# Kernel optimization log

Measured on AMD Instinct MI355X. Metric: run time of the kernel, lower is better.

## Reference

```python
import jax, jax.numpy as jnp
import numpy as np
from jax import lax

CANTOR_DEPTH = 8
VOCAB, D = 100000, 128


def setup_inputs() -> dict:
    key = jax.random.key(0)
    pentachora = jax.random.normal(key, (VOCAB, 5, D), dtype=jnp.float32)
    return {"pentachora": pentachora}


def _cantor_positions(V):
    # V: [N, 5, D]
    dt = V.dtype
    diff = V[:, :, None, :] - V[:, None, :, :]          # [N,5,5,D]
    dist_sq = jnp.sum(diff * diff, axis=-1)             # [N,5,5]
    N = V.shape[0]

    # Batched 6x6 Cayley-Menger matrix
    M = jnp.zeros((N, 6, 6), dtype=dt)
    M = M.at[:, 0, 1:].set(1.0)
    M = M.at[:, 1:, 0].set(1.0)
    M = M.at[:, 1:, 1:].set(dist_sq)
    det = jnp.linalg.det(M)                              # [N]
    volume = jnp.sqrt(jnp.clip(-det / 9216.0, 0.0))

    # Edge statistics over the 10 unique edges (torch .std() uses ddof=1)
    iu, ju = np.triu_indices(5, k=1)
    edge_lengths = jnp.sqrt(dist_sq[:, iu, ju])          # [N,10]
    mean_edge = jnp.mean(edge_lengths, axis=-1)
    std_edge = jnp.std(edge_lengths, axis=-1, ddof=1)

    # Vertex spread from centroid (ddof=1)
    centroid = jnp.mean(V, axis=1, keepdims=True)        # [N,1,D]
    cdist = jnp.linalg.norm(V - centroid, axis=-1)       # [N,5]
    spread = jnp.std(cdist, axis=-1, ddof=1)

    volume_norm = jax.nn.sigmoid(volume * 10.0)
    edge_ratio = jax.nn.sigmoid(std_edge / (mean_edge + 1e-6))
    spread_norm = jax.nn.sigmoid(spread)

    seed = jnp.clip(volume_norm * 0.4 + edge_ratio * 0.3 + spread_norm * 0.3,
                    1e-6, 1.0 - 1e-6)
    drift = (volume_norm + edge_ratio + spread_norm) * 0.01

    def step(carry, factor):
        x, cv = carry
        x_scaled = x * 3.0
        digit = jnp.floor(x_scaled)                      # x>0 so floor==trunc
        x_frac = x_scaled - digit
        cv = cv + (digit == 2.0).astype(dt) * factor
        x = jnp.clip(x_frac + drift, 1e-6, 1.0 - 1e-6)
        return (x, cv), None

    factors = (0.5 ** jnp.arange(1, CANTOR_DEPTH + 1)).astype(dt)
    (_, cantor_val), _ = lax.scan(step, (seed, jnp.zeros_like(seed)), factors)
    return jnp.clip(cantor_val, 0.0, 1.0)                # [N]


def reference(pentachora):
    return _cantor_positions(pentachora)
```

## Files before the change

kernel.cpp:

```cpp
#include <hip/hip_runtime.h>
#include <math.h>


__device__ __forceinline__ constexpr int gidx(int i, int j) {
    return i * 5 - i * (i - 1) / 2 + (j - i);
}

__global__ __launch_bounds__(256, 4) void fingerprint_kernel(
    const float* __restrict__ pent, float* __restrict__ out, int nItems)
{
    __shared__ double lds_g[32][15];

    const int tid  = threadIdx.x;
    const int wave = tid >> 6;
    const int lane = tid & 63;
    const int grp  = lane >> 3;
    const int s    = lane & 7;

    long item  = (long)blockIdx.x * 32 + (long)wave * 8 + grp;
    long itemC = item < nItems ? item : (long)nItems - 1;

    const float4* __restrict__ p =
        reinterpret_cast<const float4*>(pent + itemC * 640L);

    float4 f[5][4];
#pragma unroll
    for (int v = 0; v < 5; ++v)
#pragma unroll
        for (int j = 0; j < 4; ++j)
            f[v][j] = p[v * 32 + j * 8 + s];

    const float* fp = reinterpret_cast<const float*>(f);

    double g[15];
#pragma unroll
    for (int q = 0; q < 15; ++q) g[q] = 0.0;

#pragma unroll
    for (int t = 0; t < 16; ++t) {
        double a[5];
#pragma unroll
        for (int v = 0; v < 5; ++v)
            a[v] = (double)fp[v * 16 + t];
        int q = 0;
#pragma unroll
        for (int i = 0; i < 5; ++i)
#pragma unroll
            for (int j = i; j < 5; ++j) {
                g[q] = fma(a[i], a[j], g[q]);
                ++q;
            }
    }

#pragma unroll
    for (int m = 1; m <= 4; m <<= 1)
#pragma unroll
        for (int q = 0; q < 15; ++q) g[q] += __shfl_xor(g[q], m, 64);

    if (s == 0) {
        const int slot = wave * 8 + grp;
#pragma unroll
        for (int q = 0; q < 15; ++q) lds_g[slot][q] = g[q];
    }
    __syncthreads();

    if (tid < 32) {
        const long item2 = (long)blockIdx.x * 32 + tid;

        double h[15];
#pragma unroll
        for (int q = 0; q < 15; ++q) h[q] = lds_g[tid][q];

        double e[10];
        double se = 0.0;
        {
            int q = 0;
#pragma unroll
            for (int i = 0; i < 5; ++i)
#pragma unroll
                for (int j = i + 1; j < 5; ++j) {
                    double d2 = fma(-2.0, h[gidx(i, j)],
                                    h[gidx(i, i)] + h[gidx(j, j)]);
                    e[q] = sqrt(d2);
                    se += e[q];
                    ++q;
                }
        }
        double meanE = se * 0.1;
        double ve = 0.0;
#pragma unroll
        for (int q = 0; q < 10; ++q) {
            double d = e[q] - meanE;
            ve = fma(d, d, ve);
        }
        double stdE = sqrt(ve / 9.0);

        double S[5], T = 0.0;
#pragma unroll
        for (int i = 0; i < 5; ++i) {
            double si = 0.0;
#pragma unroll
            for (int j = 0; j < 5; ++j) {
                int a = i < j ? i : j;
                int b = i < j ? j : i;
                si += h[gidx(a, b)];
            }
            S[i] = si;
            T += si;
        }

        double scd = 0.0, cd[5];
#pragma unroll
        for (int v = 0; v < 5; ++v) {
            double c2 = fma(-0.4, S[v], h[gidx(v, v)]) + 0.04 * T;
            cd[v] = (c2 > 0.0) ? sqrt(c2) : 0.0;
            scd += cd[v];
        }
        double meanC = scd * 0.2;
        double vc = 0.0;
#pragma unroll
        for (int v = 0; v < 5; ++v) {
            double d = cd[v] - meanC;
            vc = fma(d, d, vc);
        }
        double spread = sqrt(vc * 0.25);

        double W[4][4];
#pragma unroll
        for (int pi = 0; pi < 4; ++pi)
#pragma unroll
            for (int qi = 0; qi < 4; ++qi) {
                int a0 = 0, b0 = qi + 1;
                int a1 = 0, b1 = pi + 1;
                int lo = (pi < qi ? pi : qi) + 1;
                int hi = (pi < qi ? qi : pi) + 1;
                W[pi][qi] = h[gidx(lo, hi)] - h[gidx(a0, b0)]
                          - h[gidx(a1, b1)] + h[gidx(0, 0)];
            }

        double det = 1.0;
#pragma unroll
        for (int k = 0; k < 4; ++k) {
            double pv = W[k][k];
            det *= pv;
            double inv = (pv != 0.0) ? 1.0 / pv : 0.0;
#pragma unroll
            for (int r = k + 1; r < 4; ++r) {
                double fac = W[r][k] * inv;
#pragma unroll
                for (int c = k + 1; c < 4; ++c)
                    W[r][c] = fma(-fac, W[k][c], W[r][c]);
            }
        }

        double v2 = det / 576.0;
        double volume = (v2 > 0.0) ? sqrt(v2) : 0.0;

        double vn = 1.0 / (1.0 + exp(-10.0 * volume));
        double er = 1.0 / (1.0 + exp(-(stdE / (meanE + 1e-6))));
        double sn = 1.0 / (1.0 + exp(-spread));

        double seed = 0.4 * vn + 0.3 * er + 0.3 * sn;
        seed = fmin(fmax(seed, 1e-6), 1.0 - 1e-6);
        double drift = (vn + er + sn) * 0.01;

        double x = seed, cv = 0.0, factor = 0.5;
#pragma unroll
        for (int k = 0; k < 8; ++k) {
            double xs = x * 3.0;
            double dg = floor(xs);
            double fr = xs - dg;
            cv += (dg == 2.0) ? factor : 0.0;
            factor *= 0.5;
            x = fmin(fmax(fr + drift, 1e-6), 1.0 - 1e-6);
        }
        cv = fmin(fmax(cv, 0.0), 1.0);

        if (item2 < nItems)
            out[item2] = (float)cv;
    }
}

extern "C" void kernel_launch(void* const* d_in, const int* in_sizes, int n_in,
                              void* d_out, int out_size, void* d_ws, size_t ws_size,
                              hipStream_t stream) {
    const float* pent = (const float*)d_in[0];
    float* out = (float*)d_out;
    int nItems = in_sizes[0] / 640;
    int blocks = (nItems + 31) / 32;
    hipLaunchKernelGGL(fingerprint_kernel, dim3(blocks), dim3(256), 0, stream,
                       pent, out, nItems);
}
```

Before: 45.11 us.

## Split into gram and finish kernels with transpose-reduce shuffles via workspace

Splits the fused kernel in two. The first kernel computes Gram entries, using a butterfly transpose-reduction that cuts shuffles from 45 to 14 per lane, and writes them to a column-major double workspace. The second kernel runs the scalar geometry/Cantor tail with all 256 threads active instead of 32 of 256, which removes the serialized single-wave epilogue. The cost is an extra launch and a round trip of about 12 MB of doubles through global memory. The old fused path is kept as a fallback when the workspace is too small.

New measurement: 54.85 us. +21.6%, slower.

```diff
diff --git a/kernel.cpp b/kernel.cpp
--- a/kernel.cpp
+++ b/kernel.cpp
@@ -6,11 +6,10 @@
     return i * 5 - i * (i - 1) / 2 + (j - i);
 }
 
-__global__ __launch_bounds__(256, 4) void fingerprint_kernel(
-    const float* __restrict__ pent, float* __restrict__ out, int nItems)
+__global__ __launch_bounds__(256, 6) void gram_kernel(
+    const float* __restrict__ pent, double* __restrict__ ws,
+    int nItems, int Np)
 {
-    __shared__ double lds_g[32][15];
-
     const int tid  = threadIdx.x;
     const int wave = tid >> 6;
     const int lane = tid & 63;
@@ -32,9 +31,9 @@
 
     const float* fp = reinterpret_cast<const float*>(f);
 
-    double g[15];
-#pragma unroll
-    for (int q = 0; q < 15; ++q) g[q] = 0.0;
+    double g[16];
+#pragma unroll
+    for (int q = 0; q < 16; ++q) g[q] = 0.0;
 
 #pragma unroll
     for (int t = 0; t < 16; ++t) {
@@ -52,6 +51,198 @@
             }
     }
 
+    {
+        const bool b = (s & 1) != 0;
+#pragma unroll
+        for (int i = 0; i < 8; ++i) {
+            double lo = g[i], hi = g[i + 8];
+            double recv = __shfl_xor(b ? lo : hi, 1, 64);
+            g[i] = (b ? hi : lo) + recv;
+        }
+    }
+    {
+        const bool b = (s & 2) != 0;
+#pragma unroll
+        for (int i = 0; i < 4; ++i) {
+            double lo = g[i], hi = g[i + 4];
+            double recv = __shfl_xor(b ? lo : hi, 2, 64);
+            g[i] = (b ? hi : lo) + recv;
+        }
+    }
+    {
+        const bool b = (s & 4) != 0;
+#pragma unroll
+        for (int i = 0; i < 2; ++i) {
+            double lo = g[i], hi = g[i + 2];
+            double recv = __shfl_xor(b ? lo : hi, 4, 64);
+            g[i] = (b ? hi : lo) + recv;
+        }
+    }
+    const int k = ((s & 1) << 3) | ((s & 2) << 1) | ((s & 4) >> 1);
+
+    if (item < nItems) {
+        ws[(long)k * Np + item]       = g[0];
+        ws[(long)(k + 1) * Np + item] = g[1];
+    }
+}
+
+__global__ __launch_bounds__(256) void finish_kernel(
+    const double* __restrict__ ws, float* __restrict__ out,
+    int nItems, int Np)
+{
+    const long item = (long)blockIdx.x * 256 + threadIdx.x;
+    if (item >= nItems) return;
+
+    double h[15];
+#pragma unroll
+    for (int q = 0; q < 15; ++q)
+        h[q] = ws[(long)q * Np + item];
+
+    double e[10], se = 0.0;
+    {
+        int q = 0;
+#pragma unroll
+        for (int i = 0; i < 5; ++i)
+#pragma unroll
+            for (int j = i + 1; j < 5; ++j) {
+                double d2 = fma(-2.0, h[gidx(i, j)],
+                                h[gidx(i, i)] + h[gidx(j, j)]);
+                e[q] = sqrt(d2);
+                se += e[q];
+                ++q;
+            }
+    }
+    double meanE = se * 0.1;
+    double ve = 0.0;
+#pragma unroll
+    for (int q = 0; q < 10; ++q) { double d = e[q] - meanE; ve = fma(d, d, ve); }
+    double stdE = sqrt(ve / 9.0);
+
+    double S[5], T = 0.0;
+#pragma unroll
+    for (int i = 0; i < 5; ++i) {
+        double si = 0.0;
+#pragma unroll
+        for (int j = 0; j < 5; ++j) {
+            int a = i < j ? i : j;
+            int b = i < j ? j : i;
+            si += h[gidx(a, b)];
+        }
+        S[i] = si;
+        T += si;
+    }
+
+    double scd = 0.0, cd[5];
+#pragma unroll
+    for (int v = 0; v < 5; ++v) {
+        double c2 = fma(-0.4, S[v], h[gidx(v, v)]) + 0.04 * T;
+        cd[v] = (c2 > 0.0) ? sqrt(c2) : 0.0;
+        scd += cd[v];
+    }
+    double meanC = scd * 0.2;
+    double vc = 0.0;
+#pragma unroll
+    for (int v = 0; v < 5; ++v) { double d = cd[v] - meanC; vc = fma(d, d, vc); }
+    double spread = sqrt(vc * 0.25);
+
+    double W[4][4];
+#pragma unroll
+    for (int pi = 0; pi < 4; ++pi)
+#pragma unroll
+        for (int qi = 0; qi < 4; ++qi) {
+            int lo = (pi < qi ? pi : qi) + 1;
+            int hi = (pi < qi ? qi : pi) + 1;
+            W[pi][qi] = h[gidx(lo, hi)] - h[gidx(0, qi + 1)]
+                      - h[gidx(0, pi + 1)] + h[gidx(0, 0)];
+        }
+
+    double det = 1.0;
+#pragma unroll
+    for (int kk = 0; kk < 4; ++kk) {
+        double pv = W[kk][kk];
+        det *= pv;
+        double inv = (pv != 0.0) ? 1.0 / pv : 0.0;
+#pragma unroll
+        for (int r = kk + 1; r < 4; ++r) {
+            double fac = W[r][kk] * inv;
+#pragma unroll
+            for (int c = kk + 1; c < 4; ++c)
+                W[r][c] = fma(-fac, W[kk][c], W[r][c]);
+        }
+    }
+
+    double v2 = det / 576.0;
+    double volume = (v2 > 0.0) ? sqrt(v2) : 0.0;
+
+    double vn = 1.0 / (1.0 + exp(-10.0 * volume));
+    double er = 1.0 / (1.0 + exp(-(stdE / (meanE + 1e-6))));
+    double sn = 1.0 / (1.0 + exp(-spread));
+
+    double seed = 0.4 * vn + 0.3 * er + 0.3 * sn;
+    seed = fmin(fmax(seed, 1e-6), 1.0 - 1e-6);
+    double drift = (vn + er + sn) * 0.01;
+
+    double x = seed, cv = 0.0, factor = 0.5;
+#pragma unroll
+    for (int kk = 0; kk < 8; ++kk) {
+        double xs = x * 3.0;
+        double dg = floor(xs);
+        double fr = xs - dg;
+        cv += (dg == 2.0) ? factor : 0.0;
+        factor *= 0.5;
+        x = fmin(fmax(fr + drift, 1e-6), 1.0 - 1e-6);
+    }
+    cv = fmin(fmax(cv, 0.0), 1.0);
+
+    out[item] = (float)cv;
+}
+
+__global__ __launch_bounds__(256, 4) void fused_kernel(
+    const float* __restrict__ pent, float* __restrict__ out, int nItems)
+{
+    __shared__ double lds_g[32][15];
+
+    const int tid  = threadIdx.x;
+    const int wave = tid >> 6;
+    const int lane = tid & 63;
+    const int grp  = lane >> 3;
+    const int s    = lane & 7;
+
+    long item  = (long)blockIdx.x * 32 + (long)wave * 8 + grp;
+    long itemC = item < nItems ? item : (long)nItems - 1;
+
+    const float4* __restrict__ p =
+        reinterpret_cast<const float4*>(pent + itemC * 640L);
+
+    float4 f[5][4];
+#pragma unroll
+    for (int v = 0; v < 5; ++v)
+#pragma unroll
+        for (int j = 0; j < 4; ++j)
+            f[v][j] = p[v * 32 + j * 8 + s];
+
+    const float* fp = reinterpret_cast<const float*>(f);
+
+    double g[15];
+#pragma unroll
+    for (int q = 0; q < 15; ++q) g[q] = 0.0;
+
+#pragma unroll
+    for (int t = 0; t < 16; ++t) {
+        double a[5];
+#pragma unroll
+        for (int v = 0; v < 5; ++v)
+            a[v] = (double)fp[v * 16 + t];
+        int q = 0;
+#pragma unroll
+        for (int i = 0; i < 5; ++i)
+#pragma unroll
+            for (int j = i; j < 5; ++j) {
+                g[q] = fma(a[i], a[j], g[q]);
+                ++q;
+            }
+    }
+
 #pragma unroll
     for (int m = 1; m <= 4; m <<= 1)
 #pragma unroll
@@ -71,8 +262,7 @@
 #pragma unroll
         for (int q = 0; q < 15; ++q) h[q] = lds_g[tid][q];
 
-        double e[10];
-        double se = 0.0;
+        double e[10], se = 0.0;
         {
             int q = 0;
 #pragma unroll
@@ -89,10 +279,7 @@
         double meanE = se * 0.1;
         double ve = 0.0;
 #pragma unroll
-        for (int q = 0; q < 10; ++q) {
-            double d = e[q] - meanE;
-            ve = fma(d, d, ve);
-        }
+        for (int q = 0; q < 10; ++q) { double d = e[q] - meanE; ve = fma(d, d, ve); }
         double stdE = sqrt(ve / 9.0);
 
         double S[5], T = 0.0;
@@ -119,10 +306,7 @@
         double meanC = scd * 0.2;
         double vc = 0.0;
 #pragma unroll
-        for (int v = 0; v < 5; ++v) {
-            double d = cd[v] - meanC;
-            vc = fma(d, d, vc);
-        }
+        for (int v = 0; v < 5; ++v) { double d = cd[v] - meanC; vc = fma(d, d, vc); }
         double spread = sqrt(vc * 0.25);
 
         double W[4][4];
@@ -130,26 +314,24 @@
         for (int pi = 0; pi < 4; ++pi)
 #pragma unroll
             for (int qi = 0; qi < 4; ++qi) {
-                int a0 = 0, b0 = qi + 1;
-                int a1 = 0, b1 = pi + 1;
                 int lo = (pi < qi ? pi : qi) + 1;
                 int hi = (pi < qi ? qi : pi) + 1;
-                W[pi][qi] = h[gidx(lo, hi)] - h[gidx(a0, b0)]
-                          - h[gidx(a1, b1)] + h[gidx(0, 0)];
+                W[pi][qi] = h[gidx(lo, hi)] - h[gidx(0, qi + 1)]
+                          - h[gidx(0, pi + 1)] + h[gidx(0, 0)];
             }
 
         double det = 1.0;
 #pragma unroll
-        for (int k = 0; k < 4; ++k) {
-            double pv = W[k][k];
+        for (int kk = 0; kk < 4; ++kk) {
+            double pv = W[kk][kk];
             det *= pv;
             double inv = (pv != 0.0) ? 1.0 / pv : 0.0;
 #pragma unroll
-            for (int r = k + 1; r < 4; ++r) {
-                double fac = W[r][k] * inv;
-#pragma unroll
-                for (int c = k + 1; c < 4; ++c)
-                    W[r][c] = fma(-fac, W[k][c], W[r][c]);
+            for (int r = kk + 1; r < 4; ++r) {
+                double fac = W[r][kk] * inv;
+#pragma unroll
+                for (int c = kk + 1; c < 4; ++c)
+                    W[r][c] = fma(-fac, W[kk][c], W[r][c]);
             }
         }
 
@@ -166,7 +348,7 @@
 
         double x = seed, cv = 0.0, factor = 0.5;
 #pragma unroll
-        for (int k = 0; k < 8; ++k) {
+        for (int kk = 0; kk < 8; ++kk) {
             double xs = x * 3.0;
             double dg = floor(xs);
             double fr = xs - dg;
@@ -187,7 +369,20 @@
     const float* pent = (const float*)d_in[0];
     float* out = (float*)d_out;
     int nItems = in_sizes[0] / 640;
-    int blocks = (nItems + 31) / 32;
-    hipLaunchKernelGGL(fingerprint_kernel, dim3(blocks), dim3(256), 0, stream,
-                       pent, out, nItems);
-}
+    int Np = (nItems + 255) & ~255;
+    size_t need = (size_t)16 * (size_t)Np * sizeof(double);
+
+    if (ws_size >= need) {
+        double* ws = (double*)d_ws;
+        int blocksA = (nItems + 31) / 32;
+        hipLaunchKernelGGL(gram_kernel, dim3(blocksA), dim3(256), 0, stream,
+                           pent, ws, nItems, Np);
+        int blocksB = (nItems + 255) / 256;
+        hipLaunchKernelGGL(finish_kernel, dim3(blocksB), dim3(256), 0, stream,
+                           ws, out, nItems, Np);
+    } else {
+        int blocks = (nItems + 31) / 32;
+        hipLaunchKernelGGL(fused_kernel, dim3(blocks), dim3(256), 0, stream,
+                           pent, out, nItems);
+    }
+}
```
